# Kernel tuning notes

Hardware: AMD Instinct MI355X
Metric: run time of the kernel (lower is better)

The kernel has to match this reference:

```python
import jax, jax.numpy as jnp
import numpy as np

NUM_HEADS = 8
PROJ_DIM = 64
D_MODEL = 512


def setup_inputs() -> dict:
    key = jax.random.key(0)
    ks = jax.random.split(key, 10)
    B, SQ, SK = 4, 2048, 2048
    s_in = 1.0 / np.sqrt(D_MODEL)
    s_cat = 1.0 / np.sqrt(NUM_HEADS * PROJ_DIM)
    return {
        "query_seq": jax.random.normal(ks[0], (B, SQ, D_MODEL), jnp.float32),
        "store_seq": jax.random.normal(ks[1], (B, SK, D_MODEL), jnp.float32),
        "Wq": jax.random.normal(ks[2], (NUM_HEADS, D_MODEL, PROJ_DIM), jnp.float32) * s_in,
        "bq": jnp.zeros((NUM_HEADS, PROJ_DIM), jnp.float32),
        "Wk": jax.random.normal(ks[3], (D_MODEL, PROJ_DIM), jnp.float32) * s_in,
        "bk": jnp.zeros((PROJ_DIM,), jnp.float32),
        "Wv": jax.random.normal(ks[4], (D_MODEL, PROJ_DIM), jnp.float32) * s_in,
        "bv": jnp.zeros((PROJ_DIM,), jnp.float32),
        "Wo": jax.random.normal(ks[5], (NUM_HEADS * PROJ_DIM, PROJ_DIM), jnp.float32) * s_cat,
        "bo": jnp.zeros((PROJ_DIM,), jnp.float32),
    }


def reference(query_seq, store_seq, Wq, bq, Wk, bk, Wv, bv, Wo, bo):
    # Shared K/V projections: [B, Sk, P]
    k = store_seq @ Wk + bk
    v = store_seq @ Wv + bv
    # Per-head query projections, vectorized over heads: [B, H, Sq, P]
    q = jnp.einsum("bsd,hdp->bhsp", query_seq, Wq) + bq[None, :, None, :]
    scale = 1.0 / jnp.sqrt(jnp.asarray(PROJ_DIM, jnp.float32))
    # Scores against shared K: [B, H, Sq, Sk]
    scores = jnp.einsum("bhsp,btp->bhst", q, k) * scale
    attn = jax.nn.softmax(scores, axis=-1)
    # Attend over shared V: [B, H, Sq, P]
    o = jnp.einsum("bhst,btp->bhsp", attn, v)
    B, H, SQ, P = o.shape
    concat = jnp.transpose(o, (0, 2, 1, 3)).reshape(B, SQ, H * P)
    return concat @ Wo + bo
```

## Files before the change

kernel.cpp:

```cpp
#include <hip/hip_runtime.h>
#include <math.h>

#define BATCH   4
#define SEQQ    2048
#define SEQK    2048
#define DMODEL  512
#define NHEADS  8
#define PDIM    64

#define QSCALE  0.18033688f

typedef __attribute__((ext_vector_type(8))) short short8;
typedef __attribute__((ext_vector_type(4))) float f32x4;

__device__ __forceinline__ unsigned short f2bf(float x) {
    unsigned u = __builtin_bit_cast(unsigned, x);
    u += 0x7fffu + ((u >> 16) & 1u);
    return (unsigned short)(u >> 16);
}
__device__ __forceinline__ unsigned pack_bf16_rh(float lo, float hi) {
    unsigned ul = __builtin_bit_cast(unsigned, lo) + 0x8000u;
    unsigned uh = __builtin_bit_cast(unsigned, hi) + 0x8000u;
    return __builtin_amdgcn_perm(uh, ul, 0x07060302u);
}
__device__ __forceinline__ float bf2f_lo(unsigned w) {
    return __builtin_bit_cast(float, w << 16);
}
__device__ __forceinline__ float bf2f_hi(unsigned w) {
    return __builtin_bit_cast(float, w & 0xFFFF0000u);
}
__device__ __forceinline__ float exp2_raw(float x) {
    return __builtin_amdgcn_exp2f(x);
}
__device__ __forceinline__ void glds16(const void* g, void* l) {
    __builtin_amdgcn_global_load_lds(
        (const __attribute__((address_space(1))) void*)g,
        (__attribute__((address_space(3))) void*)l, 16, 0, 0);
}

__global__ __launch_bounds__(256) void convert_w_kernel(
    const float* __restrict__ Wq, const float* __restrict__ Wk,
    const float* __restrict__ Wv, const float* __restrict__ Wo,
    unsigned short* __restrict__ Wt)
{
    const int tid = threadIdx.x;
    const int mat = blockIdx.x >> 3;
    const int k0 = (blockIdx.x & 7) << 6;
    const float sc = (mat < 8) ? QSCALE : 1.0f;
    const float* src = (mat < 8) ? (Wq + (size_t)mat * 32768)
                     : (mat == 8) ? Wk : (mat == 9) ? Wv : Wo;
    __shared__ unsigned short T[64][72];
#pragma unroll
    for (int it = 0; it < 4; ++it) {
        int flat = tid * 4 + 1024 * it;
        int k = flat >> 6, n = flat & 63;
        float4 v = *(const float4*)(src + (size_t)(k0 + k) * 64 + n);
        T[n + 0][k] = f2bf(v.x * sc);
        T[n + 1][k] = f2bf(v.y * sc);
        T[n + 2][k] = f2bf(v.z * sc);
        T[n + 3][k] = f2bf(v.w * sc);
    }
    __syncthreads();
    int n = tid >> 2, kk = (tid & 3) * 16;
    uint4 w0 = *(const uint4*)(&T[n][kk]);
    uint4 w1 = *(const uint4*)(&T[n][kk + 8]);
    *(uint4*)(Wt + (size_t)mat * 32768 + (size_t)n * 512 + k0 + kk) = w0;
    *(uint4*)(Wt + (size_t)mat * 32768 + (size_t)n * 512 + k0 + kk + 8) = w1;
}

__global__ __launch_bounds__(256, 4) void qkv_proj_kernel(
    const float* __restrict__ query, const float* __restrict__ store_,
    const unsigned short* __restrict__ Wt,
    const float* __restrict__ bq, const float* __restrict__ bk,
    const float* __restrict__ bv,
    unsigned short* __restrict__ Qbuf, unsigned short* __restrict__ Kbuf,
    unsigned short* __restrict__ Vtbuf)
{
    __shared__ unsigned short Xt[2560];
    __shared__ unsigned short Wtile[256 * 64];

    const int slot = blockIdx.y;
    const int row0 = blockIdx.x * 32;
    const int b = row0 >> 11;
    const int s0 = row0 & 2047;

    const float* X = ((slot < 2) ? query : store_) + (size_t)row0 * 512;
    const unsigned short* Wbase = Wt + (size_t)(slot * 4) * 32768;

    const int tid = threadIdx.x;
    const int wv = tid >> 6, lane = tid & 63;
    const int g = lane >> 4, c16 = lane & 15;
    const int c8 = c16 & 7;
    const int sm = wv & 1;
    const int uh = wv >> 1;
    const int lrow = lane >> 3;
    const int lcol = ((lane & 7) ^ lrow) * 8;

    f32x4 z = {0.f, 0.f, 0.f, 0.f};
    f32x4 acc[8] = {z, z, z, z, z, z, z, z};

    const int xrow = tid >> 3;
    const int xcol = (tid & 7) * 8;
    const int nwr = (slot < 2) ? 8 : 4;

    for (int k0 = 0; k0 < 512; k0 += 64) {
        float4 xa = *(const float4*)(X + (size_t)xrow * 512 + k0 + xcol);
        float4 xb = *(const float4*)(X + (size_t)xrow * 512 + k0 + xcol + 4);
        __syncthreads();
        for (int j = 0; j < nwr; ++j) {
            int rb = (nwr * wv + j) * 8;
            glds16(Wbase + (size_t)(rb + lrow) * 512 + k0 + lcol, Wtile + rb * 64);
        }
        ushort4 o0, o1;
        o0.x = f2bf(xa.x); o0.y = f2bf(xa.y); o0.z = f2bf(xa.z); o0.w = f2bf(xa.w);
        o1.x = f2bf(xb.x); o1.y = f2bf(xb.y); o1.z = f2bf(xb.z); o1.w = f2bf(xb.w);
        *(ushort4*)(&Xt[xrow * 72 + xcol]) = o0;
        *(ushort4*)(&Xt[xrow * 72 + xcol + 4]) = o1;
        __syncthreads();

        if (slot < 2) {
#pragma unroll
            for (int ks = 0; ks < 2; ++ks) {
                short8 aX = *(const short8*)(&Xt[(16 * sm + c16) * 72 + 32 * ks + 8 * g]);
#pragma unroll
                for (int uu = 0; uu < 8; ++uu) {
                    int u = 8 * uh + uu;
                    short8 bW = *(const short8*)(Wtile + (16 * u + c16) * 64 + ((4 * ks + g) ^ c8) * 8);
                    acc[uu] = __builtin_amdgcn_mfma_f32_16x16x32_bf16(aX, bW, acc[uu], 0, 0, 0);
                }
            }
        } else {
#pragma unroll
            for (int ks = 0; ks < 2; ++ks) {
                short8 aX = *(const short8*)(&Xt[(16 * sm + c16) * 72 + 32 * ks + 8 * g]);
#pragma unroll
                for (int uu = 0; uu < 4; ++uu) {
                    int u = 4 * uh + uu;
                    short8 bW = *(const short8*)(Wtile + (16 * u + c16) * 64 + ((4 * ks + g) ^ c8) * 8);
                    acc[uu] = __builtin_amdgcn_mfma_f32_16x16x32_bf16(aX, bW, acc[uu], 0, 0, 0);
                }
            }
        }
    }

    if (slot < 2) {
#pragma unroll
        for (int uu = 0; uu < 8; ++uu) {
            int u = 8 * uh + uu;
            int head = 4 * slot + (u >> 2);
            int pc = 16 * (u & 3) + c16;
            float bb = QSCALE * bq[head * 64 + pc];
            unsigned short* Y = Qbuf + ((size_t)(b * NHEADS + head) * SEQQ + s0) * PDIM;
#pragma unroll
            for (int r = 0; r < 4; ++r)
                Y[(size_t)(16 * sm + 4 * g + r) * PDIM + pc] = f2bf(acc[uu][r] + bb);
        }
    } else {
        if (uh == 0) {
            unsigned short* Yk = Kbuf + (size_t)row0 * PDIM;
#pragma unroll
            for (int uu = 0; uu < 4; ++uu) {
                float bb = bk[16 * uu + c16];
#pragma unroll
                for (int r = 0; r < 4; ++r)
                    Yk[(size_t)(16 * sm + 4 * g + r) * PDIM + 16 * uu + c16] =
                        f2bf(acc[uu][r] + bb);
            }
        }
        __syncthreads();
        if (uh == 1) {
#pragma unroll
            for (int uu = 0; uu < 4; ++uu) {
                int p = 16 * uu + c16;
                float bb = bv[p];
#pragma unroll
                for (int r = 0; r < 4; ++r)
                    Xt[p * 40 + 16 * sm + 4 * g + r] = f2bf(acc[uu][r] + bb);
            }
        }
        __syncthreads();
        int p = tid >> 2, soff = (tid & 3) * 8;
        uint4 w = *(const uint4*)(&Xt[p * 40 + soff]);
        *(uint4*)(Vtbuf + (size_t)b * PDIM * SEQK + (size_t)p * SEQK + s0 + soff) = w;
    }
}

__global__ __launch_bounds__(256, 4) void attn_kernel(
    const unsigned short* __restrict__ Qbuf,
    const unsigned short* __restrict__ Kbuf,
    const unsigned short* __restrict__ Vtbuf,
    unsigned int* __restrict__ rawO,
    float* __restrict__ Lraw)
{
    __shared__ unsigned short smem[20480];
    unsigned short* Kb = smem;
    unsigned short* Vb = smem + 8192;
    unsigned short* Ps = smem + 16384;

    const int tid = threadIdx.x;
    const int wv = tid >> 6;
    const int lane = tid & 63;
    const int g = lane >> 4;
    const int c16 = lane & 15;
    const int c8 = c16 & 7;
    const int split = blockIdx.z & 1;
    const int b = blockIdx.z >> 1;
    const int h = blockIdx.y;
    const int qt = blockIdx.x;
    const int q0 = qt * 128;

    const int lrow = lane >> 3;
    const int lcol = ((lane & 7) ^ lrow) * 8;

    const unsigned short* Qp = Qbuf + ((size_t)(b * NHEADS + h) * SEQQ + q0) * PDIM;
#pragma unroll
    for (int j = 0; j < 4; ++j) {
        int rowblk = (4 * wv + j) * 8;
        glds16(Qp + (size_t)(rowblk + lrow) * PDIM + lcol, smem + rowblk * 64);
    }
    __syncthreads();

    short8 bQ[2][2];
#pragma unroll
    for (int y = 0; y < 2; ++y)
#pragma unroll
        for (int ks = 0; ks < 2; ++ks)
            bQ[y][ks] = *(const short8*)(smem + (32 * wv + 16 * y + c16) * 64 +
                                         ((4 * ks + g) ^ c8) * 8);
    __syncthreads();

    const unsigned short* Kp  = Kbuf  + (size_t)b * SEQK * PDIM + (size_t)split * 1024 * PDIM;
    const unsigned short* Vtp = Vtbuf + (size_t)b * PDIM * SEQK + split * 1024;

#pragma unroll
    for (int j = 0; j < 2; ++j) {
        int rb = (2 * wv + j) * 8;
        glds16(Kp + (size_t)(rb + lrow) * PDIM + lcol, Kb + rb * 64);
        glds16(Vtp + (size_t)(rb + lrow) * SEQK + lcol, Vb + rb * 64);
    }

    const short one_bf = (short)0x3F80;
    short8 vones = {one_bf, one_bf, one_bf, one_bf, one_bf, one_bf, one_bf, one_bf};

    f32x4 z = {0.f, 0.f, 0.f, 0.f};
    f32x4 oacc[2][4] = {{z, z, z, z}, {z, z, z, z}};
    f32x4 lacc[2] = {z, z};
    unsigned short* PsW = Ps + wv * 1024;

    for (int i = 0; i < 16; ++i) {
        __syncthreads();
        const unsigned short* Kc = Kb + (i & 1) * 4096;
        const unsigned short* Vc = Vb + (i & 1) * 4096;
        if (i < 15) {
            int t0 = (i + 1) * 64;
            unsigned short* Kn = Kb + ((i + 1) & 1) * 4096;
            unsigned short* Vn = Vb + ((i + 1) & 1) * 4096;
#pragma unroll
            for (int j = 0; j < 2; ++j) {
                int rb = (2 * wv + j) * 8;
                glds16(Kp + (size_t)(t0 + rb + lrow) * PDIM + lcol, Kn + rb * 64);
                glds16(Vtp + (size_t)(rb + lrow) * SEQK + t0 + lcol, Vn + rb * 64);
            }
        }

        f32x4 s0a[4] = {z, z, z, z};
        f32x4 s1a[4] = {z, z, z, z};
#pragma unroll
        for (int ks = 0; ks < 2; ++ks) {
#pragma unroll
            for (int t = 0; t < 4; ++t) {
                short8 aK = *(const short8*)(Kc + (16 * t + c16) * 64 + ((4 * ks + g) ^ c8) * 8);
                s0a[t] = __builtin_amdgcn_mfma_f32_16x16x32_bf16(aK, bQ[0][ks], s0a[t], 0, 0, 0);
                s1a[t] = __builtin_amdgcn_mfma_f32_16x16x32_bf16(aK, bQ[1][ks], s1a[t], 0, 0, 0);
            }
        }

        short8 aP[2][2];
#pragma unroll
        for (int y = 0; y < 2; ++y) {
            const f32x4* sc = y ? s1a : s0a;
#pragma unroll
            for (int t = 0; t < 4; ++t) {
                float p0 = exp2_raw(sc[t][0]);
                float p1 = exp2_raw(sc[t][1]);
                float p2 = exp2_raw(sc[t][2]);
                float p3 = exp2_raw(sc[t][3]);
                uint2 w2;
                w2.x = pack_bf16_rh(p0, p1);
                w2.y = pack_bf16_rh(p2, p3);
                int phys = (2 * t + (g >> 1)) ^ c8;
                *(uint2*)(PsW + c16 * 64 + phys * 8 + 4 * (g & 1)) = w2;
            }
#pragma unroll
            for (int ks = 0; ks < 2; ++ks)
                aP[y][ks] = *(const short8*)(PsW + c16 * 64 + ((4 * ks + g) ^ c8) * 8);
        }

#pragma unroll
        for (int ks = 0; ks < 2; ++ks) {
            lacc[0] = __builtin_amdgcn_mfma_f32_16x16x32_bf16(aP[0][ks], vones, lacc[0], 0, 0, 0);
            lacc[1] = __builtin_amdgcn_mfma_f32_16x16x32_bf16(aP[1][ks], vones, lacc[1], 0, 0, 0);
#pragma unroll
            for (int u = 0; u < 4; ++u) {
                short8 bV = *(const short8*)(Vc + (16 * u + c16) * 64 + ((4 * ks + g) ^ c8) * 8);
                oacc[0][u] = __builtin_amdgcn_mfma_f32_16x16x32_bf16(aP[0][ks], bV, oacc[0][u], 0, 0, 0);
                oacc[1][u] = __builtin_amdgcn_mfma_f32_16x16x32_bf16(aP[1][ks], bV, oacc[1][u], 0, 0, 0);
            }
        }
    }

    const int rawblk = ((b * NHEADS + h) * 16 + qt) * 2 + split;
    unsigned int* rb = rawO + (size_t)rawblk * 4096;
#pragma unroll
    for (int y = 0; y < 2; ++y) {
#pragma unroll
        for (int u = 0; u < 4; ++u) {
            int slot = (wv * 2 + y) * 4 + u;
            uint2 w2;
            w2.x = pack_bf16_rh(oacc[y][u][0], oacc[y][u][1]);
            w2.y = pack_bf16_rh(oacc[y][u][2], oacc[y][u][3]);
            *(uint2*)(rb + slot * 128 + lane * 2) = w2;
        }
        if (c16 == 0) {
#pragma unroll
            for (int r = 0; r < 4; ++r)
                Lraw[(size_t)rawblk * 128 + 32 * wv + 16 * y + 4 * g + r] = lacc[y][r];
        }
    }
}

__global__ __launch_bounds__(256) void out_proj_kernel(
    const unsigned int* __restrict__ rawO, const float* __restrict__ Lraw,
    const unsigned short* __restrict__ Wt, const float* __restrict__ bo,
    float* __restrict__ out)
{
    __shared__ unsigned short XtS[32 * 264];
    __shared__ unsigned short WtS[64 * 264];

    const int tid = threadIdx.x;
    const int wv = tid >> 6, lane = tid & 63;
    const int g = lane >> 4, c16 = lane & 15;
    const int row0 = blockIdx.x * 32;
    const int b = row0 >> 11;
    const int qt = (row0 & 2047) >> 7;
    const int off = row0 & 127;
    const unsigned short* W = Wt + (size_t)10 * 32768;

    const int sm = wv & 1;
    const int uh = wv >> 1;

    f32x4 z = {0.f, 0.f, 0.f, 0.f};
    f32x4 acc[2] = {z, z};

    for (int ch = 0; ch < 2; ++ch) {
        const int h0 = 4 * ch;
        uint4 wreg[8];
        int wrow[8], wkk[8];
#pragma unroll
        for (int it = 0; it < 8; ++it) {
            int flat = tid * 8 + 2048 * it;
            wrow[it] = flat >> 8; wkk[it] = flat & 255;
            wreg[it] = *(const uint4*)(W + (size_t)wrow[it] * 512 + h0 * 64 + wkk[it]);
        }
        unsigned short vv[4][2][4];
#pragma unroll
        for (int hh = 0; hh < 4; ++hh) {
            int h = h0 + hh;
            int rb0 = ((b * NHEADS + h) * 16 + qt) * 2;
            const unsigned int* p0 = rawO + (size_t)rb0 * 4096;
            const unsigned int* p1 = rawO + (size_t)(rb0 + 1) * 4096;
            const float* l0 = Lraw + (size_t)rb0 * 128;
            const float* l1 = Lraw + (size_t)(rb0 + 1) * 128;
#pragma unroll
            for (int sl = 0; sl < 2; ++sl) {
                int s_local = 2 * wv + sl;
                int m = s_local >> 2, u = s_local & 3;
                int sglob = ((off >> 4) + m) * 4 + u;
                uint2 a0 = *(const uint2*)(p0 + sglob * 128 + lane * 2);
                uint2 a1 = *(const uint2*)(p1 + sglob * 128 + lane * 2);
                float iv[4];
#pragma unroll
                for (int r = 0; r < 4; ++r) {
                    int q = off + 16 * m + 4 * g + r;
                    iv[r] = 1.0f / (l0[q] + l1[q]);
                }
                vv[hh][sl][0] = f2bf((bf2f_lo(a0.x) + bf2f_lo(a1.x)) * iv[0]);
                vv[hh][sl][1] = f2bf((bf2f_hi(a0.x) + bf2f_hi(a1.x)) * iv[1]);
                vv[hh][sl][2] = f2bf((bf2f_lo(a0.y) + bf2f_lo(a1.y)) * iv[2]);
                vv[hh][sl][3] = f2bf((bf2f_hi(a0.y) + bf2f_hi(a1.y)) * iv[3]);
            }
        }
        __syncthreads();
#pragma unroll
        for (int it = 0; it < 8; ++it)
            *(uint4*)(&WtS[wrow[it] * 264 + wkk[it]]) = wreg[it];
#pragma unroll
        for (int hh = 0; hh < 4; ++hh)
#pragma unroll
            for (int sl = 0; sl < 2; ++sl) {
                int s_local = 2 * wv + sl;
                int m = s_local >> 2, u = s_local & 3;
#pragma unroll
                for (int r = 0; r < 4; ++r)
                    XtS[(16 * m + 4 * g + r) * 264 + hh * 64 + 16 * u + c16] = vv[hh][sl][r];
            }
        __syncthreads();

#pragma unroll
        for (int hh = 0; hh < 4; ++hh)
#pragma unroll
            for (int ks = 0; ks < 2; ++ks) {
                short8 aX = *(const short8*)(&XtS[(16 * sm + c16) * 264 + hh * 64 + 32 * ks + 8 * g]);
#pragma unroll
                for (int uu = 0; uu < 2; ++uu) {
                    int u = 2 * uh + uu;
                    short8 bW = *(const short8*)(&WtS[(16 * u + c16) * 264 + hh * 64 + 32 * ks + 8 * g]);
                    acc[uu] = __builtin_amdgcn_mfma_f32_16x16x32_bf16(aX, bW, acc[uu], 0, 0, 0);
                }
            }
    }

#pragma unroll
    for (int uu = 0; uu < 2; ++uu) {
        int u = 2 * uh + uu;
        float bb = bo[16 * u + c16];
#pragma unroll
        for (int r = 0; r < 4; ++r)
            out[(size_t)(row0 + 16 * sm + 4 * g + r) * 64 + 16 * u + c16] = acc[uu][r] + bb;
    }
}

extern "C" void kernel_launch(void* const* d_in, const int* in_sizes, int n_in,
                              void* d_out, int out_size, void* d_ws, size_t ws_size,
                              hipStream_t stream) {
    const float* query  = (const float*)d_in[0];
    const float* store_ = (const float*)d_in[1];
    const float* Wq     = (const float*)d_in[2];
    const float* bq     = (const float*)d_in[3];
    const float* Wk     = (const float*)d_in[4];
    const float* bk     = (const float*)d_in[5];
    const float* Wv     = (const float*)d_in[6];
    const float* bv     = (const float*)d_in[7];
    const float* Wo     = (const float*)d_in[8];
    const float* bo     = (const float*)d_in[9];
    float* out = (float*)d_out;

    unsigned short* Wt   = (unsigned short*)d_ws;
    unsigned short* Qbuf = Wt + (size_t)11 * 32768;
    unsigned short* Kbuf = Qbuf + (size_t)BATCH * NHEADS * SEQQ * PDIM;
    unsigned short* Vtbuf = Kbuf + (size_t)BATCH * SEQK * PDIM;
    unsigned int* rawO   = (unsigned int*)(Vtbuf + (size_t)BATCH * PDIM * SEQK);
    float* Lraw          = (float*)(rawO + (size_t)1024 * 4096);

    convert_w_kernel<<<88, 256, 0, stream>>>(Wq, Wk, Wv, Wo, Wt);

    dim3 gProj((BATCH * SEQQ) / 32, 3);
    qkv_proj_kernel<<<gProj, 256, 0, stream>>>(query, store_, Wt, bq, bk, bv,
                                               Qbuf, Kbuf, Vtbuf);

    dim3 gAttn(SEQQ / 128, NHEADS, BATCH * 2);
    attn_kernel<<<gAttn, 256, 0, stream>>>(Qbuf, Kbuf, Vtbuf, rawO, Lraw);

    out_proj_kernel<<<(BATCH * SEQQ) / 32, 256, 0, stream>>>(rawO, Lraw, Wt, bo, out);
}
```

Measured before the change: 166.9 us.

## Fuse all four stages into one persistent cooperative kernel with grid syncs

Replaces the four separate launches (weight convert, QKV projection, attention, output projection) with a single persistent cooperative kernel. Blocks loop over each stage's work items, and grid.sync() separates the stages. The goal is to remove launch gaps and tail effects between kernels. The output projection is also re-chunked to 2 heads per pass, which shrinks its shared memory so it fits within the fused kernel's single buffer. The risks are grid-sync overhead, a persistent grid sized to occupancy that may cut parallelism in the attention stage, and shared-memory and register pressure from merging all stages.

```diff
diff --git a/kernel.cpp b/kernel.cpp
--- a/kernel.cpp
+++ b/kernel.cpp
@@ -1,5 +1,8 @@
 #include <hip/hip_runtime.h>
+#include <hip/hip_cooperative_groups.h>
 #include <math.h>
+
+namespace cg = cooperative_groups;
 
 #define BATCH   4
 #define SEQQ    2048
@@ -36,6 +39,384 @@
     __builtin_amdgcn_global_load_lds(
         (const __attribute__((address_space(1))) void*)g,
         (__attribute__((address_space(3))) void*)l, 16, 0, 0);
+}
+
+__global__ __launch_bounds__(256, 4) void fused_kernel(
+    const float* __restrict__ query, const float* __restrict__ store_,
+    const float* __restrict__ Wq, const float* __restrict__ bq,
+    const float* __restrict__ Wk, const float* __restrict__ bk,
+    const float* __restrict__ Wv, const float* __restrict__ bv,
+    const float* __restrict__ Wo, const float* __restrict__ bo,
+    unsigned short* __restrict__ Wt,
+    unsigned short* __restrict__ Qbuf, unsigned short* __restrict__ Kbuf,
+    unsigned short* __restrict__ Vtbuf,
+    unsigned int* __restrict__ rawO, float* __restrict__ Lraw,
+    float* __restrict__ out)
+{
+    __shared__ unsigned short smem[18944];
+    cg::grid_group grid = cg::this_grid();
+
+    const int tid = threadIdx.x;
+    const int nblk = gridDim.x;
+    const int wv = tid >> 6;
+    const int lane = tid & 63;
+    const int g = lane >> 4;
+    const int c16 = lane & 15;
+    const int c8 = c16 & 7;
+    const int lrow = lane >> 3;
+    const int lcol = ((lane & 7) ^ lrow) * 8;
+
+    for (int w = blockIdx.x; w < 88; w += nblk) {
+        const int mat = w >> 3;
+        const int k0 = (w & 7) << 6;
+        const float sc = (mat < 8) ? QSCALE : 1.0f;
+        const float* src = (mat < 8) ? (Wq + (size_t)mat * 32768)
+                         : (mat == 8) ? Wk : (mat == 9) ? Wv : Wo;
+        unsigned short* T = smem;
+#pragma unroll
+        for (int it = 0; it < 4; ++it) {
+            int flat = tid * 4 + 1024 * it;
+            int k = flat >> 6, n = flat & 63;
+            float4 v = *(const float4*)(src + (size_t)(k0 + k) * 64 + n);
+            T[(n + 0) * 72 + k] = f2bf(v.x * sc);
+            T[(n + 1) * 72 + k] = f2bf(v.y * sc);
+            T[(n + 2) * 72 + k] = f2bf(v.z * sc);
+            T[(n + 3) * 72 + k] = f2bf(v.w * sc);
+        }
+        __syncthreads();
+        int n = tid >> 2, kk = (tid & 3) * 16;
+        uint4 w0 = *(const uint4*)(&T[n * 72 + kk]);
+        uint4 w1 = *(const uint4*)(&T[n * 72 + kk + 8]);
+        *(uint4*)(Wt + (size_t)mat * 32768 + (size_t)n * 512 + k0 + kk) = w0;
+        *(uint4*)(Wt + (size_t)mat * 32768 + (size_t)n * 512 + k0 + kk + 8) = w1;
+        __syncthreads();
+    }
+    grid.sync();
+
+    for (int w = blockIdx.x; w < 768; w += nblk) {
+        const int slot = w >> 8;
+        const int row0 = (w & 255) * 32;
+        const int b = row0 >> 11;
+        const int s0 = row0 & 2047;
+        const float* X = ((slot < 2) ? query : store_) + (size_t)row0 * 512;
+        const unsigned short* Wbase = Wt + (size_t)(slot * 4) * 32768;
+        unsigned short* Xt = smem;
+        unsigned short* Wtile = smem + 2560;
+
+        const int sm = wv & 1;
+        const int uh = wv >> 1;
+        f32x4 z = {0.f, 0.f, 0.f, 0.f};
+        f32x4 acc[8] = {z, z, z, z, z, z, z, z};
+
+        const int xrow = tid >> 3;
+        const int xcol = (tid & 7) * 8;
+        const int nwr = (slot < 2) ? 8 : 4;
+
+        for (int k0 = 0; k0 < 512; k0 += 64) {
+            float4 xa = *(const float4*)(X + (size_t)xrow * 512 + k0 + xcol);
+            float4 xb = *(const float4*)(X + (size_t)xrow * 512 + k0 + xcol + 4);
+            __syncthreads();
+            for (int j = 0; j < nwr; ++j) {
+                int rb = (nwr * wv + j) * 8;
+                glds16(Wbase + (size_t)(rb + lrow) * 512 + k0 + lcol, Wtile + rb * 64);
+            }
+            ushort4 o0, o1;
+            o0.x = f2bf(xa.x); o0.y = f2bf(xa.y); o0.z = f2bf(xa.z); o0.w = f2bf(xa.w);
+            o1.x = f2bf(xb.x); o1.y = f2bf(xb.y); o1.z = f2bf(xb.z); o1.w = f2bf(xb.w);
+            *(ushort4*)(&Xt[xrow * 72 + xcol]) = o0;
+            *(ushort4*)(&Xt[xrow * 72 + xcol + 4]) = o1;
+            __syncthreads();
+
+            if (slot < 2) {
+#pragma unroll
+                for (int ks = 0; ks < 2; ++ks) {
+                    short8 aX = *(const short8*)(&Xt[(16 * sm + c16) * 72 + 32 * ks + 8 * g]);
+#pragma unroll
+                    for (int uu = 0; uu < 8; ++uu) {
+                        int u = 8 * uh + uu;
+                        short8 bW = *(const short8*)(Wtile + (16 * u + c16) * 64 + ((4 * ks + g) ^ c8) * 8);
+                        acc[uu] = __builtin_amdgcn_mfma_f32_16x16x32_bf16(aX, bW, acc[uu], 0, 0, 0);
+                    }
+                }
+            } else {
+#pragma unroll
+                for (int ks = 0; ks < 2; ++ks) {
+                    short8 aX = *(const short8*)(&Xt[(16 * sm + c16) * 72 + 32 * ks + 8 * g]);
+#pragma unroll
+                    for (int uu = 0; uu < 4; ++uu) {
+                        int u = 4 * uh + uu;
+                        short8 bW = *(const short8*)(Wtile + (16 * u + c16) * 64 + ((4 * ks + g) ^ c8) * 8);
+                        acc[uu] = __builtin_amdgcn_mfma_f32_16x16x32_bf16(aX, bW, acc[uu], 0, 0, 0);
+                    }
+                }
+            }
+        }
+
+        if (slot < 2) {
+#pragma unroll
+            for (int uu = 0; uu < 8; ++uu) {
+                int u = 8 * uh + uu;
+                int head = 4 * slot + (u >> 2);
+                int pc = 16 * (u & 3) + c16;
+                float bb = QSCALE * bq[head * 64 + pc];
+                unsigned short* Y = Qbuf + ((size_t)(b * NHEADS + head) * SEQQ + s0) * PDIM;
+#pragma unroll
+                for (int r = 0; r < 4; ++r)
+                    Y[(size_t)(16 * sm + 4 * g + r) * PDIM + pc] = f2bf(acc[uu][r] + bb);
+            }
+        } else {
+            if (uh == 0) {
+                unsigned short* Yk = Kbuf + (size_t)row0 * PDIM;
+#pragma unroll
+                for (int uu = 0; uu < 4; ++uu) {
+                    float bb = bk[16 * uu + c16];
+#pragma unroll
+                    for (int r = 0; r < 4; ++r)
+                        Yk[(size_t)(16 * sm + 4 * g + r) * PDIM + 16 * uu + c16] =
+                            f2bf(acc[uu][r] + bb);
+                }
+            }
+            __syncthreads();
+            if (uh == 1) {
+#pragma unroll
+                for (int uu = 0; uu < 4; ++uu) {
+                    int p = 16 * uu + c16;
+                    float bb = bv[p];
+#pragma unroll
+                    for (int r = 0; r < 4; ++r)
+                        Xt[p * 40 + 16 * sm + 4 * g + r] = f2bf(acc[uu][r] + bb);
+                }
+            }
+            __syncthreads();
+            int p = tid >> 2, soff = (tid & 3) * 8;
+            uint4 wvv = *(const uint4*)(&Xt[p * 40 + soff]);
+            *(uint4*)(Vtbuf + (size_t)b * PDIM * SEQK + (size_t)p * SEQK + s0 + soff) = wvv;
+        }
+        __syncthreads();
+    }
+    grid.sync();
+
+    for (int w = blockIdx.x; w < 1024; w += nblk) {
+        const int qt = w & 15;
+        const int h = (w >> 4) & 7;
+        const int zz = w >> 7;
+        const int split = zz & 1;
+        const int b = zz >> 1;
+        const int q0 = qt * 128;
+        unsigned short* Kb = smem;
+        unsigned short* Vb = smem + 8192;
+
+        const unsigned short* Qp = Qbuf + ((size_t)(b * NHEADS + h) * SEQQ + q0) * PDIM;
+#pragma unroll
+        for (int j = 0; j < 4; ++j) {
+            int rowblk = (4 * wv + j) * 8;
+            glds16(Qp + (size_t)(rowblk + lrow) * PDIM + lcol, smem + rowblk * 64);
+        }
+        __syncthreads();
+        short8 bQ[2][2];
+#pragma unroll
+        for (int y = 0; y < 2; ++y)
+#pragma unroll
+            for (int ks = 0; ks < 2; ++ks)
+                bQ[y][ks] = *(const short8*)(smem + (32 * wv + 16 * y + c16) * 64 +
+                                             ((4 * ks + g) ^ c8) * 8);
+        __syncthreads();
+
+        const unsigned short* Kp  = Kbuf  + (size_t)b * SEQK * PDIM + (size_t)split * 1024 * PDIM;
+        const unsigned short* Vtp = Vtbuf + (size_t)b * PDIM * SEQK + split * 1024;
+#pragma unroll
+        for (int j = 0; j < 2; ++j) {
+            int rb = (2 * wv + j) * 8;
+            glds16(Kp + (size_t)(rb + lrow) * PDIM + lcol, Kb + rb * 64);
+            glds16(Vtp + (size_t)(rb + lrow) * SEQK + lcol, Vb + rb * 64);
+        }
+
+        const short one_bf = (short)0x3F80;
+        short8 vones = {one_bf, one_bf, one_bf, one_bf, one_bf, one_bf, one_bf, one_bf};
+        f32x4 z = {0.f, 0.f, 0.f, 0.f};
+        f32x4 oacc[2][4] = {{z, z, z, z}, {z, z, z, z}};
+        f32x4 lacc[2] = {z, z};
+
+        for (int i = 0; i < 16; ++i) {
+            __syncthreads();
+            unsigned short* Kc = Kb + (i & 1) * 4096;
+            const unsigned short* Vc = Vb + (i & 1) * 4096;
+            if (i < 15) {
+                int t0 = (i + 1) * 64;
+                unsigned short* Kn = Kb + ((i + 1) & 1) * 4096;
+                unsigned short* Vn = Vb + ((i + 1) & 1) * 4096;
+#pragma unroll
+                for (int j = 0; j < 2; ++j) {
+                    int rb = (2 * wv + j) * 8;
+                    glds16(Kp + (size_t)(t0 + rb + lrow) * PDIM + lcol, Kn + rb * 64);
+                    glds16(Vtp + (size_t)(rb + lrow) * SEQK + t0 + lcol, Vn + rb * 64);
+                }
+            }
+
+            f32x4 s0a[4] = {z, z, z, z};
+            f32x4 s1a[4] = {z, z, z, z};
+#pragma unroll
+            for (int ks = 0; ks < 2; ++ks) {
+#pragma unroll
+                for (int t = 0; t < 4; ++t) {
+                    short8 aK = *(const short8*)(Kc + (16 * t + c16) * 64 + ((4 * ks + g) ^ c8) * 8);
+                    s0a[t] = __builtin_amdgcn_mfma_f32_16x16x32_bf16(aK, bQ[0][ks], s0a[t], 0, 0, 0);
+                    s1a[t] = __builtin_amdgcn_mfma_f32_16x16x32_bf16(aK, bQ[1][ks], s1a[t], 0, 0, 0);
+                }
+            }
+
+            __builtin_amdgcn_s_barrier();
+            unsigned short* PsW = Kc + wv * 1024;
+
+            short8 aP[2][2];
+#pragma unroll
+            for (int y = 0; y < 2; ++y) {
+                const f32x4* sc = y ? s1a : s0a;
+#pragma unroll
+                for (int t = 0; t < 4; ++t) {
+                    float p0 = exp2_raw(sc[t][0]);
+                    float p1 = exp2_raw(sc[t][1]);
+                    float p2 = exp2_raw(sc[t][2]);
+                    float p3 = exp2_raw(sc[t][3]);
+                    uint2 w2;
+                    w2.x = pack_bf16_rh(p0, p1);
+                    w2.y = pack_bf16_rh(p2, p3);
+                    int phys = (2 * t + (g >> 1)) ^ c8;
+                    *(uint2*)(PsW + c16 * 64 + phys * 8 + 4 * (g & 1)) = w2;
+                }
+#pragma unroll
+                for (int ks = 0; ks < 2; ++ks)
+                    aP[y][ks] = *(const short8*)(PsW + c16 * 64 + ((4 * ks + g) ^ c8) * 8);
+            }
+
+#pragma unroll
+            for (int ks = 0; ks < 2; ++ks) {
+                lacc[0] = __builtin_amdgcn_mfma_f32_16x16x32_bf16(aP[0][ks], vones, lacc[0], 0, 0, 0);
+                lacc[1] = __builtin_amdgcn_mfma_f32_16x16x32_bf16(aP[1][ks], vones, lacc[1], 0, 0, 0);
+#pragma unroll
+                for (int u = 0; u < 4; ++u) {
+                    short8 bV = *(const short8*)(Vc + (16 * u + c16) * 64 + ((4 * ks + g) ^ c8) * 8);
+                    oacc[0][u] = __builtin_amdgcn_mfma_f32_16x16x32_bf16(aP[0][ks], bV, oacc[0][u], 0, 0, 0);
+                    oacc[1][u] = __builtin_amdgcn_mfma_f32_16x16x32_bf16(aP[1][ks], bV, oacc[1][u], 0, 0, 0);
+                }
+            }
+        }
+
+        const int rawblk = ((b * NHEADS + h) * 16 + qt) * 2 + split;
+        unsigned int* rbp = rawO + (size_t)rawblk * 4096;
+#pragma unroll
+        for (int y = 0; y < 2; ++y) {
+#pragma unroll
+            for (int u = 0; u < 4; ++u) {
+                int slot = (wv * 2 + y) * 4 + u;
+                uint2 w2;
+                w2.x = pack_bf16_rh(oacc[y][u][0], oacc[y][u][1]);
+                w2.y = pack_bf16_rh(oacc[y][u][2], oacc[y][u][3]);
+                *(uint2*)(rbp + slot * 128 + lane * 2) = w2;
+            }
+            if (c16 == 0) {
+#pragma unroll
+                for (int r = 0; r < 4; ++r)
+                    Lraw[(size_t)rawblk * 128 + 32 * wv + 16 * y + 4 * g + r] = lacc[y][r];
+            }
+        }
+        __syncthreads();
+    }
+    grid.sync();
+
+    for (int w = blockIdx.x; w < 256; w += nblk) {
+        unsigned short* XtS = smem;
+        unsigned short* WtS = smem + 4352;
+        const int row0 = w * 32;
+        const int b = row0 >> 11;
+        const int qt = (row0 & 2047) >> 7;
+        const int off = row0 & 127;
+        const unsigned short* W = Wt + (size_t)10 * 32768;
+        const int sm = wv & 1;
+        const int uh = wv >> 1;
+
+        f32x4 z = {0.f, 0.f, 0.f, 0.f};
+        f32x4 acc[2] = {z, z};
+
+        for (int ch = 0; ch < 4; ++ch) {
+            const int h0 = 2 * ch;
+            uint4 wreg[4];
+            int wrow[4], wkk[4];
+#pragma unroll
+            for (int it = 0; it < 4; ++it) {
+                int flat = tid * 8 + 2048 * it;
+                wrow[it] = flat >> 7; wkk[it] = flat & 127;
+                int hh = wkk[it] >> 6;
+                wreg[it] = *(const uint4*)(W + (size_t)wrow[it] * 512 + (h0 + hh) * 64 + (wkk[it] & 63));
+            }
+            unsigned short vv[2][2][4];
+#pragma unroll
+            for (int hh = 0; hh < 2; ++hh) {
+                int h = h0 + hh;
+                int rb0 = ((b * NHEADS + h) * 16 + qt) * 2;
+                const unsigned int* p0 = rawO + (size_t)rb0 * 4096;
+                const unsigned int* p1 = rawO + (size_t)(rb0 + 1) * 4096;
+                const float* l0 = Lraw + (size_t)rb0 * 128;
+                const float* l1 = Lraw + (size_t)(rb0 + 1) * 128;
+#pragma unroll
+                for (int sl = 0; sl < 2; ++sl) {
+                    int s_local = 2 * wv + sl;
+                    int m = s_local >> 2, u = s_local & 3;
+                    int sglob = ((off >> 4) + m) * 4 + u;
+                    uint2 a0 = *(const uint2*)(p0 + sglob * 128 + lane * 2);
+                    uint2 a1 = *(const uint2*)(p1 + sglob * 128 + lane * 2);
+                    float iv[4];
+#pragma unroll
+                    for (int r = 0; r < 4; ++r) {
+                        int q = off + 16 * m + 4 * g + r;
+                        iv[r] = 1.0f / (l0[q] + l1[q]);
+                    }
+                    vv[hh][sl][0] = f2bf((bf2f_lo(a0.x) + bf2f_lo(a1.x)) * iv[0]);
+                    vv[hh][sl][1] = f2bf((bf2f_hi(a0.x) + bf2f_hi(a1.x)) * iv[1]);
+                    vv[hh][sl][2] = f2bf((bf2f_lo(a0.y) + bf2f_lo(a1.y)) * iv[2]);
+                    vv[hh][sl][3] = f2bf((bf2f_hi(a0.y) + bf2f_hi(a1.y)) * iv[3]);
+                }
+            }
+            __syncthreads();
+#pragma unroll
+            for (int it = 0; it < 4; ++it)
+                *(uint4*)(&WtS[wrow[it] * 136 + wkk[it]]) = wreg[it];
+#pragma unroll
+            for (int hh = 0; hh < 2; ++hh)
+#pragma unroll
+                for (int sl = 0; sl < 2; ++sl) {
+                    int s_local = 2 * wv + sl;
+                    int m = s_local >> 2, u = s_local & 3;
+#pragma unroll
+                    for (int r = 0; r < 4; ++r)
+                        XtS[(16 * m + 4 * g + r) * 136 + hh * 64 + 16 * u + c16] = vv[hh][sl][r];
+                }
+            __syncthreads();
+
+#pragma unroll
+            for (int hh = 0; hh < 2; ++hh)
+#pragma unroll
+                for (int ks = 0; ks < 2; ++ks) {
+                    short8 aX = *(const short8*)(&XtS[(16 * sm + c16) * 136 + hh * 64 + 32 * ks + 8 * g]);
+#pragma unroll
+                    for (int uu = 0; uu < 2; ++uu) {
+                        int u = 2 * uh + uu;
+                        short8 bW = *(const short8*)(&WtS[(16 * u + c16) * 136 + hh * 64 + 32 * ks + 8 * g]);
+                        acc[uu] = __builtin_amdgcn_mfma_f32_16x16x32_bf16(aX, bW, acc[uu], 0, 0, 0);
+                    }
+                }
+        }
+
+#pragma unroll
+        for (int uu = 0; uu < 2; ++uu) {
+            int u = 2 * uh + uu;
+            float bb = bo[16 * u + c16];
+#pragma unroll
+            for (int r = 0; r < 4; ++r)
+                out[(size_t)(row0 + 16 * sm + 4 * g + r) * 64 + 16 * u + c16] = acc[uu][r] + bb;
+        }
+        __syncthreads();
+    }
 }
 
 __global__ __launch_bounds__(256) void convert_w_kernel(
@@ -83,7 +464,6 @@
     const int row0 = blockIdx.x * 32;
     const int b = row0 >> 11;
     const int s0 = row0 & 2047;
-
     const float* X = ((slot < 2) ? query : store_) + (size_t)row0 * 512;
     const unsigned short* Wbase = Wt + (size_t)(slot * 4) * 32768;
 
@@ -189,8 +569,7 @@
     const unsigned short* __restrict__ Qbuf,
     const unsigned short* __restrict__ Kbuf,
     const unsigned short* __restrict__ Vtbuf,
-    unsigned int* __restrict__ rawO,
-    float* __restrict__ Lraw)
+    unsigned int* __restrict__ rawO, float* __restrict__ Lraw)
 {
     __shared__ unsigned short smem[20480];
     unsigned short* Kb = smem;
@@ -310,7 +689,7 @@
     }
 
     const int rawblk = ((b * NHEADS + h) * 16 + qt) * 2 + split;
-    unsigned int* rb = rawO + (size_t)rawblk * 4096;
+    unsigned int* rbp = rawO + (size_t)rawblk * 4096;
 #pragma unroll
     for (int y = 0; y < 2; ++y) {
 #pragma unroll
@@ -319,7 +698,7 @@
             uint2 w2;
             w2.x = pack_bf16_rh(oacc[y][u][0], oacc[y][u][1]);
             w2.y = pack_bf16_rh(oacc[y][u][2], oacc[y][u][3]);
-            *(uint2*)(rb + slot * 128 + lane * 2) = w2;
+            *(uint2*)(rbp + slot * 128 + lane * 2) = w2;
         }
         if (c16 == 0) {
 #pragma unroll
@@ -334,8 +713,8 @@
     const unsigned short* __restrict__ Wt, const float* __restrict__ bo,
     float* __restrict__ out)
 {
-    __shared__ unsigned short XtS[32 * 264];
-    __shared__ unsigned short WtS[64 * 264];
+    __shared__ unsigned short XtS[32 * 136];
+    __shared__ unsigned short WtS[64 * 136];
 
     const int tid = threadIdx.x;
     const int wv = tid >> 6, lane = tid & 63;
@@ -345,26 +724,26 @@
     const int qt = (row0 & 2047) >> 7;
     const int off = row0 & 127;
     const unsigned short* W = Wt + (size_t)10 * 32768;
-
     const int sm = wv & 1;
     const int uh = wv >> 1;
 
     f32x4 z = {0.f, 0.f, 0.f, 0.f};
     f32x4 acc[2] = {z, z};
 
-    for (int ch = 0; ch < 2; ++ch) {
-        const int h0 = 4 * ch;
-        uint4 wreg[8];
-        int wrow[8], wkk[8];
-#pragma unroll
-        for (int it = 0; it < 8; ++it) {
+    for (int ch = 0; ch < 4; ++ch) {
+        const int h0 = 2 * ch;
+        uint4 wreg[4];
+        int wrow[4], wkk[4];
+#pragma unroll
+        for (int it = 0; it < 4; ++it) {
             int flat = tid * 8 + 2048 * it;
-            wrow[it] = flat >> 8; wkk[it] = flat & 255;
-            wreg[it] = *(const uint4*)(W + (size_t)wrow[it] * 512 + h0 * 64 + wkk[it]);
-        }
-        unsigned short vv[4][2][4];
-#pragma unroll
-        for (int hh = 0; hh < 4; ++hh) {
+            wrow[it] = flat >> 7; wkk[it] = flat & 127;
+            int hh = wkk[it] >> 6;
+            wreg[it] = *(const uint4*)(W + (size_t)wrow[it] * 512 + (h0 + hh) * 64 + (wkk[it] & 63));
+        }
+        unsigned short vv[2][2][4];
+#pragma unroll
+        for (int hh = 0; hh < 2; ++hh) {
             int h = h0 + hh;
             int rb0 = ((b * NHEADS + h) * 16 + qt) * 2;
             const unsigned int* p0 = rawO + (size_t)rb0 * 4096;
@@ -392,29 +771,29 @@
         }
         __syncthreads();
 #pragma unroll
-        for (int it = 0; it < 8; ++it)
-            *(uint4*)(&WtS[wrow[it] * 264 + wkk[it]]) = wreg[it];
-#pragma unroll
-        for (int hh = 0; hh < 4; ++hh)
+        for (int it = 0; it < 4; ++it)
+            *(uint4*)(&WtS[wrow[it] * 136 + wkk[it]]) = wreg[it];
+#pragma unroll
+        for (int hh = 0; hh < 2; ++hh)
 #pragma unroll
             for (int sl = 0; sl < 2; ++sl) {
                 int s_local = 2 * wv + sl;
                 int m = s_local >> 2, u = s_local & 3;
 #pragma unroll
                 for (int r = 0; r < 4; ++r)
-                    XtS[(16 * m + 4 * g + r) * 264 + hh * 64 + 16 * u + c16] = vv[hh][sl][r];
-            }
-        __syncthreads();
-
-#pragma unroll
-        for (int hh = 0; hh < 4; ++hh)
+                    XtS[(16 * m + 4 * g + r) * 136 + hh * 64 + 16 * u + c16] = vv[hh][sl][r];
+            }
+        __syncthreads();
+
+#pragma unroll
+        for (int hh = 0; hh < 2; ++hh)
 #pragma unroll
             for (int ks = 0; ks < 2; ++ks) {
-                short8 aX = *(const short8*)(&XtS[(16 * sm + c16) * 264 + hh * 64 + 32 * ks + 8 * g]);
+                short8 aX = *(const short8*)(&XtS[(16 * sm + c16) * 136 + hh * 64 + 32 * ks + 8 * g]);
 #pragma unroll
                 for (int uu = 0; uu < 2; ++uu) {
                     int u = 2 * uh + uu;
-                    short8 bW = *(const short8*)(&WtS[(16 * u + c16) * 264 + hh * 64 + 32 * ks + 8 * g]);
+                    short8 bW = *(const short8*)(&WtS[(16 * u + c16) * 136 + hh * 64 + 32 * ks + 8 * g]);
                     acc[uu] = __builtin_amdgcn_mfma_f32_16x16x32_bf16(aX, bW, acc[uu], 0, 0, 0);
                 }
             }
@@ -452,14 +831,30 @@
     unsigned int* rawO   = (unsigned int*)(Vtbuf + (size_t)BATCH * PDIM * SEQK);
     float* Lraw          = (float*)(rawO + (size_t)1024 * 4096);
 
-    convert_w_kernel<<<88, 256, 0, stream>>>(Wq, Wk, Wv, Wo, Wt);
-
-    dim3 gProj((BATCH * SEQQ) / 32, 3);
-    qkv_proj_kernel<<<gProj, 256, 0, stream>>>(query, store_, Wt, bq, bk, bv,
-                                               Qbuf, Kbuf, Vtbuf);
-
-    dim3 gAttn(SEQQ / 128, NHEADS, BATCH * 2);
-    attn_kernel<<<gAttn, 256, 0, stream>>>(Qbuf, Kbuf, Vtbuf, rawO, Lraw);
-
-    out_proj_kernel<<<(BATCH * SEQQ) / 32, 256, 0, stream>>>(rawO, Lraw, Wt, bo, out);
-}
+    int maxPerCU = 0;
+    hipError_t qe = hipOccupancyMaxActiveBlocksPerMultiprocessor(&maxPerCU, fused_kernel, 256, 0);
+    int nblk = 0;
+    if (qe == hipSuccess && maxPerCU >= 1) {
+        nblk = maxPerCU * 256;
+        if (nblk > 1024) nblk = 1024;
+    }
+    hipError_t le = hipErrorUnknown;
+    if (nblk >= 256) {
+        void* args[] = {(void*)&query, (void*)&store_, (void*)&Wq, (void*)&bq,
+                        (void*)&Wk, (void*)&bk, (void*)&Wv, (void*)&bv,
+                        (void*)&Wo, (void*)&bo, (void*)&Wt, (void*)&Qbuf,
+                        (void*)&Kbuf, (void*)&Vtbuf, (void*)&rawO, (void*)&Lraw,
+                        (void*)&out};
+        le = hipLaunchCooperativeKernel((void*)fused_kernel, dim3(nblk), dim3(256),
+                                        args, 0, stream);
+    }
+    if (le != hipSuccess) {
+        convert_w_kernel<<<88, 256, 0, stream>>>(Wq, Wk, Wv, Wo, Wt);
+        dim3 gProj((BATCH * SEQQ) / 32, 3);
+        qkv_proj_kernel<<<gProj, 256, 0, stream>>>(query, store_, Wt, bq, bk, bv,
+                                                   Qbuf, Kbuf, Vtbuf);
+        dim3 gAttn(SEQQ / 128, NHEADS, BATCH * 2);
+        attn_kernel<<<gAttn, 256, 0, stream>>>(Qbuf, Kbuf, Vtbuf, rawO, Lraw);
+        out_proj_kernel<<<(BATCH * SEQQ) / 32, 256, 0, stream>>>(rawO, Lraw, Wt, bo, out);
+    }
+}
```

Result: slower. 390.4 us (+133.9%).
